# Performance work log

Measured on AMD Instinct MI355X. Metric: run time of the kernel, lower is better.

The kernel has to match this reference:

```python
import jax, jax.numpy as jnp
import numpy as np

B = 131072
D = 64
H1 = 512
H2 = 256
NC = 128  # nurse classes
DC = 128  # doctor classes
EPS = 1e-5
NEG = -1e9


def _kaiming(key, fan_in, fan_out):
    # kaiming_normal_ with mode='fan_out', relu gain: std = sqrt(2/fan_out)
    return jax.random.normal(key, (fan_in, fan_out), jnp.float32) * jnp.sqrt(2.0 / fan_out)


def setup_inputs() -> dict:
    key = jax.random.key(0)
    ks = jax.random.split(key, 16)
    x = jax.random.normal(ks[0], (B, D), jnp.float32)
    sn = jax.random.randint(ks[1], (B,), 0, NC)
    sd = jax.random.randint(ks[2], (B,), 0, DC)
    # last-4 / last-3 columns carry the per-sample max class thresholds
    x = x.at[:, -4].set(sn.astype(jnp.float32)).at[:, -3].set(sd.astype(jnp.float32))
    inp = {
        'x': x,
        'W0': _kaiming(ks[3], D, H1), 'b0': jnp.zeros((H1,), jnp.float32),
        'g0': jnp.ones((H1,), jnp.float32), 'be0': jnp.zeros((H1,), jnp.float32),
        'rm0': jax.random.normal(ks[4], (H1,), jnp.float32) * 0.1,
        'rv0': jax.random.uniform(ks[5], (H1,), jnp.float32, 0.5, 1.5),
        'W1': _kaiming(ks[6], H1, H2), 'b1': jnp.zeros((H2,), jnp.float32),
        'g1': jnp.ones((H2,), jnp.float32), 'be1': jnp.zeros((H2,), jnp.float32),
        'rm1': jax.random.normal(ks[7], (H2,), jnp.float32) * 0.1,
        'rv1': jax.random.uniform(ks[8], (H2,), jnp.float32, 0.5, 1.5),
        'nW1': _kaiming(ks[9], H2, 64), 'nb1': jnp.zeros((64,), jnp.float32),
        'nW2': _kaiming(ks[10], 64, NC), 'nb2': jnp.zeros((NC,), jnp.float32),
        'dW1': _kaiming(ks[11], H2, 64), 'db1': jnp.zeros((64,), jnp.float32),
        'dW2': _kaiming(ks[12], 64, DC), 'db2': jnp.zeros((DC,), jnp.float32),
    }
    return inp


def _bn(h, g, be, rm, rv):
    # BatchNorm1d inference: normalize with running stats
    return (h - rm) * (g * jax.lax.rsqrt(rv + EPS)) + be


def reference(x, W0, b0, g0, be0, rm0, rv0, W1, b1, g1, be1, rm1, rv1,
              nW1, nb1, nW2, nb2, dW1, db1, dW2, db2):
    s_nurse = x[:, -4].astype(jnp.int32)   # [B]
    s_doctor = x[:, -3].astype(jnp.int32)  # [B]

    h = jax.nn.relu(_bn(x @ W0 + b0, g0, be0, rm0, rv0))   # [B,H1]
    h = jax.nn.relu(_bn(h @ W1 + b1, g1, be1, rm1, rv1))   # [B,H2]

    nurse_logits = jax.nn.relu(h @ nW1 + nb1) @ nW2 + nb2   # [B,NC]
    doctor_logits = jax.nn.relu(h @ dW1 + db1) @ dW2 + db2  # [B,DC]

    # vectorized range mask: positions <= s_max are kept
    nmask = (jnp.arange(NC)[None, :] <= s_nurse[:, None]).astype(nurse_logits.dtype)
    dmask = (jnp.arange(DC)[None, :] <= s_doctor[:, None]).astype(doctor_logits.dtype)
    nurse_logits = nurse_logits * nmask + (1.0 - nmask) * NEG
    doctor_logits = doctor_logits * dmask + (1.0 - dmask) * NEG
    return (nurse_logits, doctor_logits)
```

## Files before the change

### kernel.cpp

```cpp
#include <hip/hip_runtime.h>

#define NB 131072
#define NEG9 -1e9f

typedef __attribute__((ext_vector_type(8))) __bf16 bf16x8;
typedef __attribute__((ext_vector_type(4))) float f32x4;
typedef __attribute__((ext_vector_type(4))) unsigned short u16x4;

__device__ __forceinline__ f32x4 mfma16(bf16x8 a, bf16x8 b, f32x4 c) {
    return __builtin_amdgcn_mfma_f32_16x16x32_bf16(a, b, c, 0, 0, 0);
}

__device__ __forceinline__ unsigned short f2bf(float f) {
    unsigned u = __builtin_bit_cast(unsigned, f);
    u += 0x7fffu + ((u >> 16) & 1u);
    return (unsigned short)(u >> 16);
}

struct __align__(16) Wspace {
    unsigned short W0t[512][64];
    unsigned short W1t[256][512];
    unsigned short nW1t[64][256];
    unsigned short dW1t[64][256];
    unsigned short nW2t[128][64];
    unsigned short dW2t[128][64];
    float c0[512];
    float c1[256];
    float nb1c[64], db1c[64];
    float nb2c[128], db2c[128];
};

__device__ Wspace g_ws;

__global__ void prep_kernel(
    const float* __restrict__ W0, const float* __restrict__ b0,
    const float* __restrict__ g0, const float* __restrict__ be0,
    const float* __restrict__ rm0, const float* __restrict__ rv0,
    const float* __restrict__ W1, const float* __restrict__ b1,
    const float* __restrict__ g1, const float* __restrict__ be1,
    const float* __restrict__ rm1, const float* __restrict__ rv1,
    const float* __restrict__ nW1, const float* __restrict__ nb1,
    const float* __restrict__ nW2, const float* __restrict__ nb2,
    const float* __restrict__ dW1, const float* __restrict__ db1,
    const float* __restrict__ dW2, const float* __restrict__ db2)
{
    const int tid = blockIdx.x * 256 + threadIdx.x;

    {
        int n = tid >> 9, k = tid & 511;
        float s = g1[n] * rsqrtf(rv1[n] + 1e-5f);
        ((unsigned short*)g_ws.W1t)[tid] = f2bf(W1[k * 256 + n] * s);
    }
    if (tid < 512 * 64) {
        int n = tid >> 6, k = tid & 63;
        float s = g0[n] * rsqrtf(rv0[n] + 1e-5f);
        ((unsigned short*)g_ws.W0t)[tid] = f2bf(W0[k * 512 + n] * s);
    }
    if (tid < 64 * 256) {
        int n = tid >> 8, k = tid & 255;
        ((unsigned short*)g_ws.nW1t)[tid] = f2bf(nW1[k * 64 + n]);
        ((unsigned short*)g_ws.dW1t)[tid] = f2bf(dW1[k * 64 + n]);
    }
    if (tid < 128 * 64) {
        int n = tid >> 6, k = tid & 63;
        ((unsigned short*)g_ws.nW2t)[tid] = f2bf(nW2[k * 128 + n]);
        ((unsigned short*)g_ws.dW2t)[tid] = f2bf(dW2[k * 128 + n]);
    }
    if (tid < 512) g_ws.c0[tid] = (b0[tid] - rm0[tid]) * (g0[tid] * rsqrtf(rv0[tid] + 1e-5f)) + be0[tid];
    if (tid < 256) g_ws.c1[tid] = (b1[tid] - rm1[tid]) * (g1[tid] * rsqrtf(rv1[tid] + 1e-5f)) + be1[tid];
    if (tid < 64) { g_ws.nb1c[tid] = nb1[tid]; g_ws.db1c[tid] = db1[tid]; }
    if (tid < 128) { g_ws.nb2c[tid] = nb2[tid]; g_ws.db2c[tid] = db2[tid]; }
}

__global__ __launch_bounds__(256, 3) void fused_mlp(
    const float4* __restrict__ x4, float* __restrict__ out)
{
    __shared__ __align__(16) unsigned short sXs[64 * 72];
    __shared__ __align__(16) unsigned short sH0[64 * 264];
    __shared__ __align__(16) unsigned short sAd[64 * 72];
    __shared__ int scl[2][64];

    const int tid = threadIdx.x;
    const int w = tid >> 6;
    const int lane = tid & 63;
    const int m = lane & 15;
    const int q = lane >> 4;
    const int row0 = blockIdx.x * 64;

    for (int i = tid; i < 64 * 16; i += 256) {
        int r = i >> 4, c4 = i & 15;
        float4 v = x4[(size_t)(row0 + r) * 16 + c4];
        u16x4 p = { f2bf(v.x), f2bf(v.y), f2bf(v.z), f2bf(v.w) };
        *(u16x4*)&sXs[r * 72 + c4 * 4] = p;
        if (c4 == 15) { scl[0][r] = (int)v.x; scl[1][r] = (int)v.y; }
    }
    __syncthreads();

    f32x4 acc1[4][4];
#pragma unroll
    for (int a = 0; a < 4; ++a)
#pragma unroll
        for (int b = 0; b < 4; ++b) acc1[a][b] = f32x4{0.f, 0.f, 0.f, 0.f};

    for (int ch = 0; ch < 2; ++ch) {
#pragma unroll
        for (int nt = 0; nt < 4; ++nt) {
            const int col = ch * 256 + w * 64 + nt * 16 + m;
            const int lc = w * 64 + nt * 16 + m;
            bf16x8 b0 = *(const bf16x8*)&g_ws.W0t[col][q * 8];
            bf16x8 b1 = *(const bf16x8*)&g_ws.W0t[col][32 + q * 8];
            float bias = g_ws.c0[col];
#pragma unroll
            for (int mt = 0; mt < 4; ++mt) {
                bf16x8 a0 = *(const bf16x8*)&sXs[(mt * 16 + m) * 72 + q * 8];
                bf16x8 a1 = *(const bf16x8*)&sXs[(mt * 16 + m) * 72 + 32 + q * 8];
                f32x4 c = {0.f, 0.f, 0.f, 0.f};
                c = mfma16(a0, b0, c);
                c = mfma16(a1, b1, c);
#pragma unroll
                for (int r = 0; r < 4; ++r)
                    sH0[(mt * 16 + q * 4 + r) * 264 + lc] = f2bf(fmaxf(c[r] + bias, 0.f));
            }
        }
        __syncthreads();

#pragma unroll
        for (int ks = 0; ks < 8; ++ks) {
            const int k0 = ks * 32;
            bf16x8 bfr[4], afr[4];
#pragma unroll
            for (int nt = 0; nt < 4; ++nt)
                bfr[nt] = *(const bf16x8*)&g_ws.W1t[w * 64 + nt * 16 + m][ch * 256 + k0 + q * 8];
#pragma unroll
            for (int mt = 0; mt < 4; ++mt)
                afr[mt] = *(const bf16x8*)&sH0[(mt * 16 + m) * 264 + k0 + q * 8];
#pragma unroll
            for (int nt = 0; nt < 4; ++nt)
#pragma unroll
                for (int mt = 0; mt < 4; ++mt)
                    acc1[nt][mt] = mfma16(afr[mt], bfr[nt], acc1[nt][mt]);
        }
        __syncthreads();
    }

#pragma unroll
    for (int nt = 0; nt < 4; ++nt) {
        const int col = w * 64 + nt * 16 + m;
        float bias = g_ws.c1[col];
#pragma unroll
        for (int mt = 0; mt < 4; ++mt)
#pragma unroll
            for (int r = 0; r < 4; ++r)
                sH0[(mt * 16 + q * 4 + r) * 264 + col] = f2bf(fmaxf(acc1[nt][mt][r] + bias, 0.f));
    }
    __syncthreads();

    {
        const int head = w >> 1;
        const unsigned short (*Wh)[256] = head ? g_ws.dW1t : g_ws.nW1t;
        const float* bh = head ? g_ws.db1c : g_ws.nb1c;
        unsigned short* Ah = head ? sAd : sXs;
        f32x4 acc[2][4];
#pragma unroll
        for (int a = 0; a < 2; ++a)
#pragma unroll
            for (int b = 0; b < 4; ++b) acc[a][b] = f32x4{0.f, 0.f, 0.f, 0.f};
#pragma unroll
        for (int ks = 0; ks < 8; ++ks) {
            const int k0 = ks * 32;
            bf16x8 bfr[2], afr[4];
#pragma unroll
            for (int nt = 0; nt < 2; ++nt)
                bfr[nt] = *(const bf16x8*)&Wh[(w & 1) * 32 + nt * 16 + m][k0 + q * 8];
#pragma unroll
            for (int mt = 0; mt < 4; ++mt)
                afr[mt] = *(const bf16x8*)&sH0[(mt * 16 + m) * 264 + k0 + q * 8];
#pragma unroll
            for (int nt = 0; nt < 2; ++nt)
#pragma unroll
                for (int mt = 0; mt < 4; ++mt)
                    acc[nt][mt] = mfma16(afr[mt], bfr[nt], acc[nt][mt]);
        }
#pragma unroll
        for (int nt = 0; nt < 2; ++nt) {
            const int col = (w & 1) * 32 + nt * 16 + m;
            float bias = bh[col];
#pragma unroll
            for (int mt = 0; mt < 4; ++mt)
#pragma unroll
                for (int r = 0; r < 4; ++r)
                    Ah[(mt * 16 + q * 4 + r) * 72 + col] = f2bf(fmaxf(acc[nt][mt][r] + bias, 0.f));
        }
    }
    __syncthreads();

    {
        const int head = w >> 1;
        const unsigned short (*W2)[64] = head ? g_ws.dW2t : g_ws.nW2t;
        const float* b2 = head ? g_ws.db2c : g_ws.nb2c;
        const unsigned short* Ah = head ? sAd : sXs;
        const int* sc = scl[head];
        float* op = out + (size_t)head * (size_t)NB * 128;

        bf16x8 a0f[4], a1f[4];
#pragma unroll
        for (int mt = 0; mt < 4; ++mt) {
            a0f[mt] = *(const bf16x8*)&Ah[(mt * 16 + m) * 72 + q * 8];
            a1f[mt] = *(const bf16x8*)&Ah[(mt * 16 + m) * 72 + 32 + q * 8];
        }
#pragma unroll
        for (int ct = 0; ct < 4; ++ct) {
            const int col = (w & 1) * 64 + ct * 16 + m;
            bf16x8 b0 = *(const bf16x8*)&W2[col][q * 8];
            bf16x8 b1 = *(const bf16x8*)&W2[col][32 + q * 8];
            float bias = b2[col];
#pragma unroll
            for (int mt = 0; mt < 4; ++mt) {
                f32x4 c = {0.f, 0.f, 0.f, 0.f};
                c = mfma16(a0f[mt], b0, c);
                c = mfma16(a1f[mt], b1, c);
#pragma unroll
                for (int r = 0; r < 4; ++r) {
                    const int row = mt * 16 + q * 4 + r;
                    float v = c[r] + bias;
                    v = (col <= sc[row]) ? v : NEG9;
                    op[(size_t)(row0 + row) * 128 + col] = v;
                }
            }
        }
    }
}

extern "C" void kernel_launch(void* const* d_in, const int* in_sizes, int n_in,
                              void* d_out, int out_size, void* d_ws, size_t ws_size,
                              hipStream_t stream) {
    (void)in_sizes; (void)n_in; (void)d_ws; (void)ws_size;

    prep_kernel<<<512, 256, 0, stream>>>(
        (const float*)d_in[1], (const float*)d_in[2], (const float*)d_in[3],
        (const float*)d_in[4], (const float*)d_in[5], (const float*)d_in[6],
        (const float*)d_in[7], (const float*)d_in[8], (const float*)d_in[9],
        (const float*)d_in[10], (const float*)d_in[11], (const float*)d_in[12],
        (const float*)d_in[13], (const float*)d_in[14], (const float*)d_in[15],
        (const float*)d_in[16], (const float*)d_in[17], (const float*)d_in[18],
        (const float*)d_in[19], (const float*)d_in[20]);

    fused_mlp<<<NB / 64, 256, 0, stream>>>((const float4*)d_in[0], (float*)d_out);
}
```

Baseline: 292.3 us.

## Swap MFMA operand order and use k-grouped LDS layout with vectorized packed stores

Swaps the MFMA operands so weights are the A operand and activations the B operand. Each lane's accumulator then holds four consecutive output columns of one row, which allows packed bf16x4 LDS writes via perm and float4 global stores in place of scalar ones. Activations are re-laid out in LDS as k-groups of 8 (group, row, 8) to cut footprint, and occupancy goes up to 4 blocks per CU. Both heads now share the same hidden-fragment reads, each wave computing 16 columns of each head, and the mask thresholds are read straight from global memory. The risks are extra register pressure from the higher launch bound, and possible LDS bank conflicts in the new layout.

Result: slower. 321.2 us (+9.9%).

```diff
diff --git a/kernel.cpp b/kernel.cpp
--- a/kernel.cpp
+++ b/kernel.cpp
@@ -5,10 +5,16 @@
 
 typedef __attribute__((ext_vector_type(8))) __bf16 bf16x8;
 typedef __attribute__((ext_vector_type(4))) float f32x4;
-typedef __attribute__((ext_vector_type(4))) unsigned short u16x4;
+typedef __attribute__((ext_vector_type(2))) unsigned int u32x2;
+typedef __attribute__((ext_vector_type(4))) unsigned int u32x4;
 
 __device__ __forceinline__ f32x4 mfma16(bf16x8 a, bf16x8 b, f32x4 c) {
     return __builtin_amdgcn_mfma_f32_16x16x32_bf16(a, b, c, 0, 0, 0);
+}
+
+__device__ __forceinline__ unsigned pk(float h, float l) {
+    return __builtin_amdgcn_perm(__builtin_bit_cast(unsigned, h),
+                                 __builtin_bit_cast(unsigned, l), 0x07060302u);
 }
 
 __device__ __forceinline__ unsigned short f2bf(float f) {
@@ -72,27 +78,29 @@
     if (tid < 128) { g_ws.nb2c[tid] = nb2[tid]; g_ws.db2c[tid] = db2[tid]; }
 }
 
-__global__ __launch_bounds__(256, 3) void fused_mlp(
+__global__ __launch_bounds__(256, 4) void fused_mlp(
     const float4* __restrict__ x4, float* __restrict__ out)
 {
-    __shared__ __align__(16) unsigned short sXs[64 * 72];
-    __shared__ __align__(16) unsigned short sH0[64 * 264];
-    __shared__ __align__(16) unsigned short sAd[64 * 72];
-    __shared__ int scl[2][64];
-
+    __shared__ __align__(16) unsigned short sBig[32 * 64 * 8];
+    __shared__ __align__(16) unsigned short sXs[8 * 64 * 8];
+
+    const float* xf = (const float*)x4;
     const int tid = threadIdx.x;
     const int w = tid >> 6;
     const int lane = tid & 63;
     const int m = lane & 15;
     const int q = lane >> 4;
+    const int qh = q >> 1;
+    const int ql = (q & 1) * 4;
     const int row0 = blockIdx.x * 64;
 
-    for (int i = tid; i < 64 * 16; i += 256) {
-        int r = i >> 4, c4 = i & 15;
-        float4 v = x4[(size_t)(row0 + r) * 16 + c4];
-        u16x4 p = { f2bf(v.x), f2bf(v.y), f2bf(v.z), f2bf(v.w) };
-        *(u16x4*)&sXs[r * 72 + c4 * 4] = p;
-        if (c4 == 15) { scl[0][r] = (int)v.x; scl[1][r] = (int)v.y; }
+    for (int it = 0; it < 2; ++it) {
+        int i = it * 256 + tid;
+        int g = i & 7, r = i >> 3;
+        float4 v0 = x4[(size_t)(row0 + r) * 16 + g * 2];
+        float4 v1 = x4[(size_t)(row0 + r) * 16 + g * 2 + 1];
+        u32x4 p = { pk(v0.y, v0.x), pk(v0.w, v0.z), pk(v1.y, v1.x), pk(v1.w, v1.z) };
+        *(u32x4*)&sXs[(g * 64 + r) * 8] = p;
     }
     __syncthreads();
 
@@ -105,127 +113,127 @@
     for (int ch = 0; ch < 2; ++ch) {
 #pragma unroll
         for (int nt = 0; nt < 4; ++nt) {
-            const int col = ch * 256 + w * 64 + nt * 16 + m;
-            const int lc = w * 64 + nt * 16 + m;
-            bf16x8 b0 = *(const bf16x8*)&g_ws.W0t[col][q * 8];
-            bf16x8 b1 = *(const bf16x8*)&g_ws.W0t[col][32 + q * 8];
-            float bias = g_ws.c0[col];
+            const int gcb = ch * 256 + w * 64 + nt * 16;
+            bf16x8 wa0 = *(const bf16x8*)&g_ws.W0t[gcb + m][q * 8];
+            bf16x8 wa1 = *(const bf16x8*)&g_ws.W0t[gcb + m][32 + q * 8];
+            f32x4 bias = *(const f32x4*)&g_ws.c0[gcb + q * 4];
+            const int lgb = w * 8 + nt * 2 + qh;
 #pragma unroll
             for (int mt = 0; mt < 4; ++mt) {
-                bf16x8 a0 = *(const bf16x8*)&sXs[(mt * 16 + m) * 72 + q * 8];
-                bf16x8 a1 = *(const bf16x8*)&sXs[(mt * 16 + m) * 72 + 32 + q * 8];
+                bf16x8 xq0 = *(const bf16x8*)&sXs[(q * 64 + mt * 16 + m) * 8];
+                bf16x8 xq1 = *(const bf16x8*)&sXs[((4 + q) * 64 + mt * 16 + m) * 8];
                 f32x4 c = {0.f, 0.f, 0.f, 0.f};
-                c = mfma16(a0, b0, c);
-                c = mfma16(a1, b1, c);
-#pragma unroll
-                for (int r = 0; r < 4; ++r)
-                    sH0[(mt * 16 + q * 4 + r) * 264 + lc] = f2bf(fmaxf(c[r] + bias, 0.f));
+                c = mfma16(wa0, xq0, c);
+                c = mfma16(wa1, xq1, c);
+                u32x2 pw = { pk(fmaxf(c[1] + bias[1], 0.f), fmaxf(c[0] + bias[0], 0.f)),
+                             pk(fmaxf(c[3] + bias[3], 0.f), fmaxf(c[2] + bias[2], 0.f)) };
+                *(u32x2*)&sBig[(lgb * 64 + mt * 16 + m) * 8 + ql] = pw;
             }
         }
         __syncthreads();
 
 #pragma unroll
         for (int ks = 0; ks < 8; ++ks) {
-            const int k0 = ks * 32;
-            bf16x8 bfr[4], afr[4];
+            bf16x8 wb[4], ab[4];
 #pragma unroll
             for (int nt = 0; nt < 4; ++nt)
-                bfr[nt] = *(const bf16x8*)&g_ws.W1t[w * 64 + nt * 16 + m][ch * 256 + k0 + q * 8];
+                wb[nt] = *(const bf16x8*)&g_ws.W1t[w * 64 + nt * 16 + m][ch * 256 + ks * 32 + q * 8];
 #pragma unroll
             for (int mt = 0; mt < 4; ++mt)
-                afr[mt] = *(const bf16x8*)&sH0[(mt * 16 + m) * 264 + k0 + q * 8];
+                ab[mt] = *(const bf16x8*)&sBig[((ks * 4 + q) * 64 + mt * 16 + m) * 8];
 #pragma unroll
             for (int nt = 0; nt < 4; ++nt)
 #pragma unroll
                 for (int mt = 0; mt < 4; ++mt)
-                    acc1[nt][mt] = mfma16(afr[mt], bfr[nt], acc1[nt][mt]);
+                    acc1[nt][mt] = mfma16(wb[nt], ab[mt], acc1[nt][mt]);
         }
         __syncthreads();
     }
 
 #pragma unroll
     for (int nt = 0; nt < 4; ++nt) {
-        const int col = w * 64 + nt * 16 + m;
-        float bias = g_ws.c1[col];
-#pragma unroll
-        for (int mt = 0; mt < 4; ++mt)
-#pragma unroll
-            for (int r = 0; r < 4; ++r)
-                sH0[(mt * 16 + q * 4 + r) * 264 + col] = f2bf(fmaxf(acc1[nt][mt][r] + bias, 0.f));
+        const int cb = w * 64 + nt * 16;
+        f32x4 bias = *(const f32x4*)&g_ws.c1[cb + q * 4];
+        const int gb = (cb >> 3) + qh;
+#pragma unroll
+        for (int mt = 0; mt < 4; ++mt) {
+            f32x4 c = acc1[nt][mt];
+            u32x2 pw = { pk(fmaxf(c[1] + bias[1], 0.f), fmaxf(c[0] + bias[0], 0.f)),
+                         pk(fmaxf(c[3] + bias[3], 0.f), fmaxf(c[2] + bias[2], 0.f)) };
+            *(u32x2*)&sBig[(gb * 64 + mt * 16 + m) * 8 + ql] = pw;
+        }
+    }
+    __syncthreads();
+
+    f32x4 aN[4], aD[4];
+#pragma unroll
+    for (int b = 0; b < 4; ++b) { aN[b] = f32x4{0.f, 0.f, 0.f, 0.f}; aD[b] = f32x4{0.f, 0.f, 0.f, 0.f}; }
+#pragma unroll
+    for (int ks = 0; ks < 8; ++ks) {
+        bf16x8 wn = *(const bf16x8*)&g_ws.nW1t[w * 16 + m][ks * 32 + q * 8];
+        bf16x8 wd = *(const bf16x8*)&g_ws.dW1t[w * 16 + m][ks * 32 + q * 8];
+#pragma unroll
+        for (int mt = 0; mt < 4; ++mt) {
+            bf16x8 ab = *(const bf16x8*)&sBig[((ks * 4 + q) * 64 + mt * 16 + m) * 8];
+            aN[mt] = mfma16(wn, ab, aN[mt]);
+            aD[mt] = mfma16(wd, ab, aD[mt]);
+        }
     }
     __syncthreads();
 
     {
-        const int head = w >> 1;
-        const unsigned short (*Wh)[256] = head ? g_ws.dW1t : g_ws.nW1t;
-        const float* bh = head ? g_ws.db1c : g_ws.nb1c;
-        unsigned short* Ah = head ? sAd : sXs;
-        f32x4 acc[2][4];
-#pragma unroll
-        for (int a = 0; a < 2; ++a)
-#pragma unroll
-            for (int b = 0; b < 4; ++b) acc[a][b] = f32x4{0.f, 0.f, 0.f, 0.f};
-#pragma unroll
-        for (int ks = 0; ks < 8; ++ks) {
-            const int k0 = ks * 32;
-            bf16x8 bfr[2], afr[4];
-#pragma unroll
-            for (int nt = 0; nt < 2; ++nt)
-                bfr[nt] = *(const bf16x8*)&Wh[(w & 1) * 32 + nt * 16 + m][k0 + q * 8];
-#pragma unroll
-            for (int mt = 0; mt < 4; ++mt)
-                afr[mt] = *(const bf16x8*)&sH0[(mt * 16 + m) * 264 + k0 + q * 8];
-#pragma unroll
-            for (int nt = 0; nt < 2; ++nt)
-#pragma unroll
-                for (int mt = 0; mt < 4; ++mt)
-                    acc[nt][mt] = mfma16(afr[mt], bfr[nt], acc[nt][mt]);
-        }
-#pragma unroll
-        for (int nt = 0; nt < 2; ++nt) {
-            const int col = (w & 1) * 32 + nt * 16 + m;
-            float bias = bh[col];
-#pragma unroll
-            for (int mt = 0; mt < 4; ++mt)
-#pragma unroll
-                for (int r = 0; r < 4; ++r)
-                    Ah[(mt * 16 + q * 4 + r) * 72 + col] = f2bf(fmaxf(acc[nt][mt][r] + bias, 0.f));
-        }
-    }
-    __syncthreads();
-
-    {
-        const int head = w >> 1;
+        f32x4 bn = *(const f32x4*)&g_ws.nb1c[w * 16 + q * 4];
+        f32x4 bd = *(const f32x4*)&g_ws.db1c[w * 16 + q * 4];
+        const int gn = w * 2 + qh;
+#pragma unroll
+        for (int mt = 0; mt < 4; ++mt) {
+            f32x4 c = aN[mt];
+            u32x2 pw = { pk(fmaxf(c[1] + bn[1], 0.f), fmaxf(c[0] + bn[0], 0.f)),
+                         pk(fmaxf(c[3] + bn[3], 0.f), fmaxf(c[2] + bn[2], 0.f)) };
+            *(u32x2*)&sBig[(gn * 64 + mt * 16 + m) * 8 + ql] = pw;
+            c = aD[mt];
+            u32x2 pd = { pk(fmaxf(c[1] + bd[1], 0.f), fmaxf(c[0] + bd[0], 0.f)),
+                         pk(fmaxf(c[3] + bd[3], 0.f), fmaxf(c[2] + bd[2], 0.f)) };
+            *(u32x2*)&sBig[((8 + gn) * 64 + mt * 16 + m) * 8 + ql] = pd;
+        }
+    }
+    __syncthreads();
+
+    int thrN[4], thrD[4];
+#pragma unroll
+    for (int mt = 0; mt < 4; ++mt) {
+        size_t rb = (size_t)(row0 + mt * 16 + m) * 64;
+        thrN[mt] = (int)xf[rb + 60];
+        thrD[mt] = (int)xf[rb + 61];
+    }
+#pragma unroll
+    for (int head = 0; head < 2; ++head) {
         const unsigned short (*W2)[64] = head ? g_ws.dW2t : g_ws.nW2t;
         const float* b2 = head ? g_ws.db2c : g_ws.nb2c;
-        const unsigned short* Ah = head ? sAd : sXs;
-        const int* sc = scl[head];
+        const int gbase = head ? 8 : 0;
+        const int* thr = head ? thrD : thrN;
         float* op = out + (size_t)head * (size_t)NB * 128;
-
-        bf16x8 a0f[4], a1f[4];
-#pragma unroll
-        for (int mt = 0; mt < 4; ++mt) {
-            a0f[mt] = *(const bf16x8*)&Ah[(mt * 16 + m) * 72 + q * 8];
-            a1f[mt] = *(const bf16x8*)&Ah[(mt * 16 + m) * 72 + 32 + q * 8];
-        }
-#pragma unroll
-        for (int ct = 0; ct < 4; ++ct) {
-            const int col = (w & 1) * 64 + ct * 16 + m;
-            bf16x8 b0 = *(const bf16x8*)&W2[col][q * 8];
-            bf16x8 b1 = *(const bf16x8*)&W2[col][32 + q * 8];
-            float bias = b2[col];
+#pragma unroll
+        for (int ct = 0; ct < 2; ++ct) {
+            const int cb = w * 32 + ct * 16;
+            bf16x8 w0 = *(const bf16x8*)&W2[cb + m][q * 8];
+            bf16x8 w1 = *(const bf16x8*)&W2[cb + m][32 + q * 8];
+            f32x4 bias = *(const f32x4*)&b2[cb + q * 4];
 #pragma unroll
             for (int mt = 0; mt < 4; ++mt) {
+                bf16x8 a0 = *(const bf16x8*)&sBig[((gbase + q) * 64 + mt * 16 + m) * 8];
+                bf16x8 a1 = *(const bf16x8*)&sBig[((gbase + 4 + q) * 64 + mt * 16 + m) * 8];
                 f32x4 c = {0.f, 0.f, 0.f, 0.f};
-                c = mfma16(a0f[mt], b0, c);
-                c = mfma16(a1f[mt], b1, c);
-#pragma unroll
-                for (int r = 0; r < 4; ++r) {
-                    const int row = mt * 16 + q * 4 + r;
-                    float v = c[r] + bias;
-                    v = (col <= sc[row]) ? v : NEG9;
-                    op[(size_t)(row0 + row) * 128 + col] = v;
-                }
+                c = mfma16(w0, a0, c);
+                c = mfma16(w1, a1, c);
+                const int ci = cb + q * 4;
+                const int t = thr[mt];
+                float4 v;
+                v.x = (ci + 0 <= t) ? c[0] + bias[0] : NEG9;
+                v.y = (ci + 1 <= t) ? c[1] + bias[1] : NEG9;
+                v.z = (ci + 2 <= t) ? c[2] + bias[2] : NEG9;
+                v.w = (ci + 3 <= t) ? c[3] + bias[3] : NEG9;
+                *(float4*)&op[(size_t)(row0 + mt * 16 + m) * 128 + ci] = v;
             }
         }
     }
```
